# Performance work log

Hardware: AMD Instinct MI355X
Metric: run time of the kernel (lower is better)

The kernel has to match this reference:

```python
import math
import jax, jax.numpy as jnp
import numpy as np

T = 2048       # sequence_length
H = 2048       # hidden_size
NH = 32        # num_attention_heads
NKV = 8        # num_key_value_heads
HD = 64        # head_dim
SW = 128       # sliding_window
QM = NH // NKV # q_mult (GQA group size)
ROPE_THETA = 10000.0
EPS = 1e-5


def setup_inputs() -> dict:
    key = jax.random.key(0)
    k_x, k_s, k_qkv, k_out = jax.random.split(key, 4)
    x = jax.random.normal(k_x, (T, H), dtype=jnp.float32)
    scale = jnp.ones((H,), dtype=jnp.float32)
    sinks = jax.random.normal(k_s, (NH,), dtype=jnp.float32) * 0.02
    qkv_dim = HD * (NH + 2 * NKV)  # 3072
    qkv_kernel = jax.random.normal(k_qkv, (H, qkv_dim), dtype=jnp.float32) * (1.0 / math.sqrt(H))
    qkv_bias = jnp.zeros((qkv_dim,), dtype=jnp.float32)
    out_kernel = jax.random.normal(k_out, (H, H), dtype=jnp.float32) * (1.0 / math.sqrt(H))
    out_bias = jnp.zeros((H,), dtype=jnp.float32)
    # RoPE tables: [T, HD//2]
    half = HD // 2
    inv_freq = 1.0 / (ROPE_THETA ** (np.arange(half, dtype=np.float64) / half))
    ang = np.outer(np.arange(T, dtype=np.float64), inv_freq)
    cos_table = jnp.asarray(np.cos(ang), dtype=jnp.float32)
    sin_table = jnp.asarray(np.sin(ang), dtype=jnp.float32)
    # causal + sliding-window additive mask [T, T]
    qp = np.arange(T, dtype=np.int32)[:, None]
    kp = np.arange(T, dtype=np.int32)[None, :]
    m = np.where(kp > qp, -np.inf, 0.0) + np.where(qp - kp > SW, -np.inf, 0.0)
    mask = jnp.asarray(m, dtype=jnp.float32)
    return dict(x=x, scale=scale, sinks=sinks, qkv_kernel=qkv_kernel,
                qkv_bias=qkv_bias, out_kernel=out_kernel, out_bias=out_bias,
                cos_table=cos_table, sin_table=sin_table, mask=mask)


def _rmsnorm(x, scale):
    t = x.astype(jnp.float32)
    rms = jnp.sqrt(jnp.mean(t * t, axis=-1, keepdims=True) + EPS)
    return ((t / rms) * scale).astype(x.dtype)


def _rope(x, cos, sin):
    # x: [T, ..., HD]; split-half rotation as in the reference RotaryEmbedding
    shp = x.shape
    xr = x.reshape(shp[0], -1, HD)
    c = cos[:, None, :].astype(xr.dtype)
    s = sin[:, None, :].astype(xr.dtype)
    x1, x2 = jnp.split(xr, 2, axis=-1)
    y = jnp.concatenate([x1 * c - x2 * s, x2 * c + x1 * s], axis=-1)
    return y.reshape(shp)


def reference(x, scale, sinks, qkv_kernel, qkv_bias, out_kernel, out_bias,
              cos_table, sin_table, mask):
    normed = _rmsnorm(x, scale)
    qkv = normed @ qkv_kernel + qkv_bias                 # [T, 3072]
    q_end = NH * HD
    k_end = q_end + NKV * HD
    q = qkv[:, :q_end].reshape(T, NKV, QM, HD)           # [T, nkv, qm, hd]
    k = qkv[:, q_end:k_end].reshape(T, NKV, HD)          # [T, nkv, hd]
    v = qkv[:, k_end:].reshape(T, NKV, HD)               # [T, nkv, hd]
    q = _rope(q, cos_table, sin_table)
    k = _rope(k, cos_table, sin_table)
    sm_scale = 1.0 / math.sqrt(float(HD))
    # GQA attention without materializing repeated K/V
    logits = jnp.einsum('qnmd,knd->nmqk', q, k) * sm_scale  # [nkv, qm, T, T]
    logits = logits + mask[None, None, :, :]
    sink_col = jnp.broadcast_to(sinks.reshape(NKV, QM, 1, 1), (NKV, QM, T, 1))
    logits = jnp.concatenate([logits, sink_col], axis=-1)   # [nkv, qm, T, T+1]
    weights = jax.nn.softmax(logits, axis=-1)[..., :-1]     # drop sink column
    attn = jnp.einsum('nmqk,knd->qnmd', weights, v).reshape(T, NH * HD)
    projected = attn @ out_kernel + out_bias
    return x + projected
```

## Files before the change

### kernel.cpp

```cpp
#include <hip/hip_runtime.h>
#include <hip/hip_bf16.h>
#include <stdint.h>

typedef __bf16 bf16_t;
typedef __attribute__((ext_vector_type(8))) __bf16 bf16x8;
typedef __attribute__((ext_vector_type(4))) __bf16 bf16x4;
typedef __attribute__((ext_vector_type(4))) float f32x4;

static constexpr int T_SEQ = 2048;
static constexpr int HID   = 2048;
static constexpr int NHEAD = 32;
static constexpr int NKVH  = 8;
static constexpr int HDIM  = 64;
static constexpr int QKVD  = 3072;

__device__ inline f32x4 mfma16(bf16x8 a, bf16x8 b, f32x4 c) {
    return __builtin_amdgcn_mfma_f32_16x16x32_bf16(a, b, c, 0, 0, 0);
}

__device__ inline void load_lds16(const bf16_t* g, bf16_t* l) {
    __builtin_amdgcn_global_load_lds(
        (const __attribute__((address_space(1))) void*)g,
        (__attribute__((address_space(3))) void*)l, 16, 0, 0);
}

__global__ __launch_bounds__(256) void prep_kernel(const float* __restrict__ Wq,
                                                   const float* __restrict__ Wo,
                                                   bf16_t* __restrict__ Tq,
                                                   bf16_t* __restrict__ To,
                                                   const float* __restrict__ x,
                                                   const float* __restrict__ scale,
                                                   bf16_t* __restrict__ normed,
                                                   const float* __restrict__ obias,
                                                   float* __restrict__ out) {
    __shared__ float tile[64 * 65];
    int b = blockIdx.x;
    const int t = threadIdx.x;
    if (b < 2560) {
        const float* in; bf16_t* outw; int NN, KK, bx, by;
        if (b < 1536) { in = Wq; outw = Tq; NN = QKVD; KK = HID; bx = b % 48; by = b / 48; }
        else { b -= 1536; in = Wo; outw = To; NN = HID; KK = HID; bx = b % 32; by = b / 32; }
        const int c4 = (t & 15) * 4;
#pragma unroll
        for (int i = 0; i < 4; ++i) {
            int r = (t >> 4) + i * 16;
            float4 v = *(const float4*)(in + (size_t)(by*64 + r) * NN + bx*64 + c4);
            tile[r*65 + c4 + 0] = v.x; tile[r*65 + c4 + 1] = v.y;
            tile[r*65 + c4 + 2] = v.z; tile[r*65 + c4 + 3] = v.w;
        }
        __syncthreads();
        const int kc = t & 7;
#pragma unroll
        for (int i = 0; i < 2; ++i) {
            int n = (t >> 3) + i * 32;
            bf16x8 o;
#pragma unroll
            for (int j = 0; j < 8; ++j) o[j] = (bf16_t)tile[(kc*8 + j)*65 + n];
            *(bf16x8*)(outw + (size_t)(bx*64 + n) * KK + by*64 + kc*8) = o;
        }
    } else {
        int row = b - 2560;
        const float4* x4 = (const float4*)(x + (size_t)row * HID);
        const float4* s4 = (const float4*)scale;
        const float4* b4 = (const float4*)obias;
        float4 v0 = x4[t], v1 = x4[t + 256];
        float ss = v0.x*v0.x + v0.y*v0.y + v0.z*v0.z + v0.w*v0.w
                 + v1.x*v1.x + v1.y*v1.y + v1.z*v1.z + v1.w*v1.w;
#pragma unroll
        for (int off = 32; off > 0; off >>= 1) ss += __shfl_down(ss, off);
        if ((t & 63) == 0) tile[t >> 6] = ss;
        __syncthreads();
        float total = tile[0] + tile[1] + tile[2] + tile[3];
        float inv = rsqrtf(total * (1.0f / HID) + 1e-5f);
        float4 sc0 = s4[t], sc1 = s4[t + 256];
        bf16_t* outr = normed + (size_t)row * HID;
        bf16x4 o0, o1;
        o0.x = (bf16_t)(v0.x*inv*sc0.x); o0.y = (bf16_t)(v0.y*inv*sc0.y);
        o0.z = (bf16_t)(v0.z*inv*sc0.z); o0.w = (bf16_t)(v0.w*inv*sc0.w);
        o1.x = (bf16_t)(v1.x*inv*sc1.x); o1.y = (bf16_t)(v1.y*inv*sc1.y);
        o1.z = (bf16_t)(v1.z*inv*sc1.z); o1.w = (bf16_t)(v1.w*inv*sc1.w);
        *(bf16x4*)(outr + 4*t)        = o0;
        *(bf16x4*)(outr + 1024 + 4*t) = o1;
        float4 bb0 = b4[t], bb1 = b4[t + 256];
        float4 oi0 = {v0.x + bb0.x, v0.y + bb0.y, v0.z + bb0.z, v0.w + bb0.w};
        float4 oi1 = {v1.x + bb1.x, v1.y + bb1.y, v1.z + bb1.z, v1.w + bb1.w};
        float* orow = out + (size_t)row * HID;
        *(float4*)(orow + 4*t)        = oi0;
        *(float4*)(orow + 1024 + 4*t) = oi1;
    }
}

template <int ATOMIC>
__global__ __launch_bounds__(256) void gemm_splitk(const bf16_t* __restrict__ A,
                                                   const bf16_t* __restrict__ Bt,
                                                   bf16_t* __restrict__ Cpart,
                                                   float* __restrict__ Cred,
                                                   int M, int N, int K) {
    __shared__ __align__(16) bf16_t Asm[2 * 128 * 32];
    __shared__ __align__(16) bf16_t Bsm[2 * 128 * 32];
    const int tid = threadIdx.x;
    const int bm = blockIdx.y * 128, bn = blockIdx.x * 128;
    const int kh = K >> 1;
    const int kb = blockIdx.z * kh;
    const int lane = tid & 63, wave = tid >> 6;
    const int wm = (wave & 1) * 64, wn = (wave >> 1) * 64;
    const int lm = lane & 15, quad = lane >> 4;

    f32x4 acc[4][4];
#pragma unroll
    for (int i = 0; i < 4; ++i)
#pragma unroll
        for (int j = 0; j < 4; ++j) acc[i][j] = (f32x4){0.f, 0.f, 0.f, 0.f};

    const int cid0 = tid, cid1 = tid + 256;
    const int r0 = cid0 >> 2, c0 = (cid0 & 3) ^ ((r0 >> 1) & 3);
    const int r1 = cid1 >> 2, c1 = (cid1 & 3) ^ ((r1 >> 1) & 3);
    const bf16_t* Ab = A  + (size_t)bm * K + kb;
    const bf16_t* Bb = Bt + (size_t)bn * K + kb;
    const size_t ga0 = (size_t)r0 * K + c0 * 8;
    const size_t ga1 = (size_t)r1 * K + c1 * 8;
    bf16_t* ldsA0a = &Asm[wave * 512];
    bf16_t* ldsA0b = &Asm[2048 + wave * 512];
    bf16_t* ldsA1a = &Asm[4096 + wave * 512];
    bf16_t* ldsA1b = &Asm[4096 + 2048 + wave * 512];
    bf16_t* ldsB0a = &Bsm[wave * 512];
    bf16_t* ldsB0b = &Bsm[2048 + wave * 512];
    bf16_t* ldsB1a = &Bsm[4096 + wave * 512];
    bf16_t* ldsB1b = &Bsm[4096 + 2048 + wave * 512];
    const int swz = (quad ^ ((lm >> 1) & 3)) * 8;

    for (int k0 = 0; k0 < kh; k0 += 64) {
        load_lds16(Ab + ga0 + k0,      ldsA0a);
        load_lds16(Ab + ga1 + k0,      ldsA0b);
        load_lds16(Ab + ga0 + k0 + 32, ldsA1a);
        load_lds16(Ab + ga1 + k0 + 32, ldsA1b);
        load_lds16(Bb + ga0 + k0,      ldsB0a);
        load_lds16(Bb + ga1 + k0,      ldsB0b);
        load_lds16(Bb + ga0 + k0 + 32, ldsB1a);
        load_lds16(Bb + ga1 + k0 + 32, ldsB1b);
        __syncthreads();
#pragma unroll
        for (int ks = 0; ks < 2; ++ks) {
            bf16x8 af[4], bfr[4];
#pragma unroll
            for (int i = 0; i < 4; ++i)
                af[i]  = *(const bf16x8*)&Asm[ks*4096 + (wm + i*16 + lm)*32 + swz];
#pragma unroll
            for (int j = 0; j < 4; ++j)
                bfr[j] = *(const bf16x8*)&Bsm[ks*4096 + (wn + j*16 + lm)*32 + swz];
#pragma unroll
            for (int i = 0; i < 4; ++i)
#pragma unroll
                for (int j = 0; j < 4; ++j) acc[i][j] = mfma16(af[i], bfr[j], acc[i][j]);
        }
        __syncthreads();
    }

    if (ATOMIC) {
#pragma unroll
        for (int i = 0; i < 4; ++i) {
            int gr = bm + wm + i*16 + quad*4;
#pragma unroll
            for (int j = 0; j < 4; ++j) {
                int gc = bn + wn + j*16 + lm;
#pragma unroll
                for (int r = 0; r < 4; ++r)
                    atomicAdd(&Cred[(size_t)(gr + r)*N + gc], acc[i][j][r]);
            }
        }
    } else {
        bf16_t* Cp = Cpart + (size_t)blockIdx.z * M * N;
#pragma unroll
        for (int i = 0; i < 4; ++i) {
            int gr = bm + wm + i*16 + quad*4;
#pragma unroll
            for (int j = 0; j < 4; ++j) {
                int gc = bn + wn + j*16 + lm;
#pragma unroll
                for (int r = 0; r < 4; ++r)
                    Cp[(size_t)(gr + r)*N + gc] = (bf16_t)acc[i][j][r];
            }
        }
    }
}

__global__ __launch_bounds__(192) void rope_split(const bf16_t* __restrict__ qp0,
                                                  const bf16_t* __restrict__ qp1,
                                                  const float* __restrict__ qbias,
                                                  const float* __restrict__ cost,
                                                  const float* __restrict__ sint,
                                                  bf16_t* __restrict__ Qb,
                                                  bf16_t* __restrict__ Kb,
                                                  bf16_t* __restrict__ Vb) {
    const int t = blockIdx.x;
    const int hr = threadIdx.x >> 2, p0 = (threadIdx.x & 3) * 8;
    const bf16_t* r0 = qp0 + (size_t)t * QKVD + hr * 64;
    const bf16_t* r1 = qp1 + (size_t)t * QKVD + hr * 64;
    bf16x8 a1 = *(const bf16x8*)(r0 + p0);
    bf16x8 a2 = *(const bf16x8*)(r0 + p0 + 32);
    bf16x8 b1 = *(const bf16x8*)(r1 + p0);
    bf16x8 b2 = *(const bf16x8*)(r1 + p0 + 32);
    const float* qb = qbias + hr * 64;
    float x1[8], x2[8];
#pragma unroll
    for (int j = 0; j < 8; ++j) {
        x1[j] = (float)a1[j] + (float)b1[j] + qb[p0 + j];
        x2[j] = (float)a2[j] + (float)b2[j] + qb[p0 + j + 32];
    }
    bf16x8 w1, w2;
    if (hr < 40) {
        const float* c = cost + (size_t)t * 32 + p0;
        const float* s = sint + (size_t)t * 32 + p0;
#pragma unroll
        for (int j = 0; j < 8; ++j) {
            float cc = c[j], ss = s[j];
            w1[j] = (bf16_t)(x1[j]*cc - x2[j]*ss);
            w2[j] = (bf16_t)(x2[j]*cc + x1[j]*ss);
        }
    } else {
#pragma unroll
        for (int j = 0; j < 8; ++j) { w1[j] = (bf16_t)x1[j]; w2[j] = (bf16_t)x2[j]; }
    }
    bf16_t* dst;
    if (hr < 32)      dst = Qb + ((size_t)t*NHEAD + hr)      * HDIM;
    else if (hr < 40) dst = Kb + ((size_t)t*NKVH + (hr-32))  * HDIM;
    else              dst = Vb + ((size_t)t*NKVH + (hr-40))  * HDIM;
    *(bf16x8*)(dst + p0)      = w1;
    *(bf16x8*)(dst + p0 + 32) = w2;
}

__global__ __launch_bounds__(256) void attn_kernel(const bf16_t* __restrict__ Qb,
                                                   const bf16_t* __restrict__ Kb,
                                                   const bf16_t* __restrict__ Vb,
                                                   const float* __restrict__ sinks,
                                                   bf16_t* __restrict__ attnb) {
    __shared__ __align__(16) bf16_t Vt[64 * 200];
    __shared__ __align__(16) bf16_t Ws[64 * 200];

    const int tid = threadIdx.x;
    const int qt = blockIdx.x, h = blockIdx.y;
    const int qs = qt * 64;
    const int nkv = h >> 2;

    {
        const int off = (tid >> 5) * 8;
#pragma unroll
        for (int it = 0; it < 3; ++it) {
            int j2 = (tid & 31) + 32 * it;
            int kg0 = qs - 128 + 2*j2;     if (kg0 < 0) kg0 = 0;
            int kg1 = qs - 128 + 2*j2 + 1; if (kg1 < 0) kg1 = 0;
            union { uint4 u; bf16_t e[8]; } v0, v1;
            v0.u = *(const uint4*)(Vb + ((size_t)kg0*NKVH + nkv)*HDIM + off);
            v1.u = *(const uint4*)(Vb + ((size_t)kg1*NKVH + nkv)*HDIM + off);
#pragma unroll
            for (int r = 0; r < 8; ++r) {
                union { uint u; bf16_t e[2]; } p;
                p.e[0] = v0.e[r]; p.e[1] = v1.e[r];
                *(uint*)&Vt[(off + r)*200 + 2*j2] = p.u;
            }
        }
    }

    const int lane = tid & 63, wave = tid >> 6;
    const int lm = lane & 15, quad = lane >> 4;
    const int w16 = wave * 16;

    f32x4 S[12];
#pragma unroll
    for (int jt = 0; jt < 12; ++jt) S[jt] = (f32x4){0.f, 0.f, 0.f, 0.f};
    const bf16_t* Qrow = Qb + ((size_t)(qs + w16 + lm)*NHEAD + h)*HDIM + quad*8;
    int krow[12];
#pragma unroll
    for (int jt = 0; jt < 12; ++jt) {
        int kg = qs - 128 + jt*16 + lm;
        krow[jt] = kg < 0 ? 0 : kg;
    }
#pragma unroll
    for (int ks = 0; ks < 2; ++ks) {
        bf16x8 aq = *(const bf16x8*)(Qrow + ks*32);
#pragma unroll
        for (int jt = 0; jt < 12; ++jt) {
            bf16x8 bk = *(const bf16x8*)(Kb + ((size_t)krow[jt]*NKVH + nkv)*HDIM + ks*32 + quad*8);
            S[jt] = mfma16(aq, bk, S[jt]);
        }
    }

    const float sink = sinks[h];
#pragma unroll
    for (int reg = 0; reg < 4; ++reg) {
        const int qg = qs + w16 + quad*4 + reg;
        float mx = -1e30f;
#pragma unroll
        for (int jt = 0; jt < 12; ++jt) {
            int kg = qs - 128 + jt*16 + lm;
            float sv = S[jt][reg] * 0.125f;
            bool valid = (kg >= 0) && (kg <= qg) && (qg - kg <= 128);
            sv = valid ? sv : -1e30f;
            S[jt][reg] = sv;
            mx = fmaxf(mx, sv);
        }
#pragma unroll
        for (int off = 1; off < 16; off <<= 1) mx = fmaxf(mx, __shfl_xor(mx, off));
        float M = fmaxf(mx, sink);
        float sum = 0.f;
#pragma unroll
        for (int jt = 0; jt < 12; ++jt) {
            float e = __expf(S[jt][reg] - M);
            S[jt][reg] = e; sum += e;
        }
#pragma unroll
        for (int off = 1; off < 16; off <<= 1) sum += __shfl_xor(sum, off);
        float rden = 1.f / (sum + __expf(sink - M));
#pragma unroll
        for (int jt = 0; jt < 12; ++jt)
            Ws[(w16 + quad*4 + reg)*200 + jt*16 + lm] = (bf16_t)(S[jt][reg] * rden);
    }
    __syncthreads();

    f32x4 O[4];
#pragma unroll
    for (int nt = 0; nt < 4; ++nt) O[nt] = (f32x4){0.f, 0.f, 0.f, 0.f};
#pragma unroll
    for (int ks = 0; ks < 6; ++ks) {
        bf16x8 aw = *(const bf16x8*)&Ws[(w16 + lm)*200 + ks*32 + quad*8];
#pragma unroll
        for (int nt = 0; nt < 4; ++nt) {
            bf16x8 bv = *(const bf16x8*)&Vt[(nt*16 + lm)*200 + ks*32 + quad*8];
            O[nt] = mfma16(aw, bv, O[nt]);
        }
    }
#pragma unroll
    for (int nt = 0; nt < 4; ++nt)
#pragma unroll
        for (int reg = 0; reg < 4; ++reg)
            attnb[(size_t)(qs + w16 + quad*4 + reg)*HID + h*HDIM + nt*16 + lm] =
                (bf16_t)(O[nt][reg]);
}

extern "C" void kernel_launch(void* const* d_in, const int* in_sizes, int n_in,
                              void* d_out, int out_size, void* d_ws, size_t ws_size,
                              hipStream_t stream) {
    (void)in_sizes; (void)n_in; (void)out_size; (void)ws_size;
    const float* x          = (const float*)d_in[0];
    const float* scale      = (const float*)d_in[1];
    const float* sinks      = (const float*)d_in[2];
    const float* qkv_kernel = (const float*)d_in[3];
    const float* qkv_bias   = (const float*)d_in[4];
    const float* out_kernel = (const float*)d_in[5];
    const float* out_bias   = (const float*)d_in[6];
    const float* cos_t      = (const float*)d_in[7];
    const float* sin_t      = (const float*)d_in[8];
    float* out = (float*)d_out;

    char* ws = (char*)d_ws;
    const size_t MiB = 1048576;
    bf16_t* Wt_out = (bf16_t*)(ws);
    bf16_t* Wt_qkv = (bf16_t*)(ws + 8*MiB);
    bf16_t* attnb  = (bf16_t*)(ws + 8*MiB);
    bf16_t* normed = (bf16_t*)(ws + 20*MiB);
    bf16_t* qkvp   = (bf16_t*)(ws + 28*MiB);
    bf16_t* Qb     = (bf16_t*)(ws + 52*MiB);
    bf16_t* Kb     = (bf16_t*)(ws + 60*MiB);
    bf16_t* Vb     = (bf16_t*)(ws + 62*MiB);

    prep_kernel<<<4608, 256, 0, stream>>>(qkv_kernel, out_kernel, Wt_qkv, Wt_out,
                                          x, scale, normed, out_bias, out);
    gemm_splitk<0><<<dim3(QKVD/128, T_SEQ/128, 2), 256, 0, stream>>>(normed, Wt_qkv, qkvp,
                                                                     nullptr, T_SEQ, QKVD, HID);
    rope_split<<<T_SEQ, 192, 0, stream>>>(qkvp, qkvp + (size_t)T_SEQ*QKVD, qkv_bias,
                                          cos_t, sin_t, Qb, Kb, Vb);
    attn_kernel<<<dim3(T_SEQ/64, NHEAD), 256, 0, stream>>>(Qb, Kb, Vb, sinks, attnb);
    gemm_splitk<1><<<dim3(HID/128, T_SEQ/128, 2), 256, 0, stream>>>(attnb, Wt_out, nullptr,
                                                                    out, T_SEQ, HID, HID);
}
```

Measured before the change: 231.2 us.

## Fuse split-K reduction with RoPE/bias epilogues via per-tile flag handoff

```diff
diff --git a/kernel.cpp b/kernel.cpp
--- a/kernel.cpp
+++ b/kernel.cpp
@@ -23,6 +23,59 @@
         (const __attribute__((address_space(1))) void*)g,
         (__attribute__((address_space(3))) void*)l, 16, 0, 0);
 }
+
+#define GEMM_CORE(A_, Bt_, K_)                                                      \
+    const int tid = threadIdx.x;                                                    \
+    const int bm = blockIdx.y * 128, bn = blockIdx.x * 128;                         \
+    const int kh = (K_) >> 1;                                                       \
+    const int kb = blockIdx.z * kh;                                                 \
+    const int lane = tid & 63, wave = tid >> 6;                                     \
+    const int wm = (wave & 1) * 64, wn = (wave >> 1) * 64;                          \
+    const int lm = lane & 15, quad = lane >> 4;                                     \
+    f32x4 acc[4][4];                                                                \
+    _Pragma("unroll") for (int i = 0; i < 4; ++i)                                   \
+        _Pragma("unroll") for (int j = 0; j < 4; ++j)                               \
+            acc[i][j] = (f32x4){0.f, 0.f, 0.f, 0.f};                                \
+    {                                                                               \
+        const int cid0 = tid, cid1 = tid + 256;                                     \
+        const int r0 = cid0 >> 2, c0 = (cid0 & 3) ^ ((r0 >> 1) & 3);                \
+        const int r1 = cid1 >> 2, c1 = (cid1 & 3) ^ ((r1 >> 1) & 3);                \
+        const bf16_t* Ab = (A_)  + (size_t)bm * (K_) + kb;                          \
+        const bf16_t* Bb = (Bt_) + (size_t)bn * (K_) + kb;                          \
+        const size_t ga0 = (size_t)r0 * (K_) + c0 * 8;                              \
+        const size_t ga1 = (size_t)r1 * (K_) + c1 * 8;                              \
+        bf16_t* lA0a = &Asm[wave * 512];                                            \
+        bf16_t* lA0b = &Asm[2048 + wave * 512];                                     \
+        bf16_t* lA1a = &Asm[4096 + wave * 512];                                     \
+        bf16_t* lA1b = &Asm[6144 + wave * 512];                                     \
+        bf16_t* lB0a = &Bsm[wave * 512];                                            \
+        bf16_t* lB0b = &Bsm[2048 + wave * 512];                                     \
+        bf16_t* lB1a = &Bsm[4096 + wave * 512];                                     \
+        bf16_t* lB1b = &Bsm[6144 + wave * 512];                                     \
+        const int swz = (quad ^ ((lm >> 1) & 3)) * 8;                               \
+        for (int k0 = 0; k0 < kh; k0 += 64) {                                       \
+            load_lds16(Ab + ga0 + k0,      lA0a);                                   \
+            load_lds16(Ab + ga1 + k0,      lA0b);                                   \
+            load_lds16(Ab + ga0 + k0 + 32, lA1a);                                   \
+            load_lds16(Ab + ga1 + k0 + 32, lA1b);                                   \
+            load_lds16(Bb + ga0 + k0,      lB0a);                                   \
+            load_lds16(Bb + ga1 + k0,      lB0b);                                   \
+            load_lds16(Bb + ga0 + k0 + 32, lB1a);                                   \
+            load_lds16(Bb + ga1 + k0 + 32, lB1b);                                   \
+            __syncthreads();                                                        \
+            _Pragma("unroll") for (int ks = 0; ks < 2; ++ks) {                      \
+                bf16x8 af[4], bfr[4];                                               \
+                _Pragma("unroll") for (int i = 0; i < 4; ++i)                       \
+                    af[i]  = *(const bf16x8*)&Asm[ks*4096 + (wm + i*16 + lm)*32 + swz]; \
+                _Pragma("unroll") for (int j = 0; j < 4; ++j)                       \
+                    bfr[j] = *(const bf16x8*)&Bsm[ks*4096 + (wn + j*16 + lm)*32 + swz]; \
+                _Pragma("unroll") for (int i = 0; i < 4; ++i)                       \
+                    _Pragma("unroll") for (int j = 0; j < 4; ++j)                   \
+                        acc[i][j] = mfma16(af[i], bfr[j], acc[i][j]);               \
+            }                                                                       \
+            __syncthreads();                                                        \
+        }                                                                           \
+    }
 
 __global__ __launch_bounds__(256) void prep_kernel(const float* __restrict__ Wq,
                                                    const float* __restrict__ Wo,
@@ -31,11 +84,14 @@
                                                    const float* __restrict__ x,
                                                    const float* __restrict__ scale,
                                                    bf16_t* __restrict__ normed,
-                                                   const float* __restrict__ obias,
-                                                   float* __restrict__ out) {
+                                                   unsigned* __restrict__ flags) {
     __shared__ float tile[64 * 65];
     int b = blockIdx.x;
     const int t = threadIdx.x;
+    if (b == 4608) {
+        for (int i = t; i < 640; i += 256) flags[i] = 0u;
+        return;
+    }
     if (b < 2560) {
         const float* in; bf16_t* outw; int NN, KK, bx, by;
         if (b < 1536) { in = Wq; outw = Tq; NN = QKVD; KK = HID; bx = b % 48; by = b / 48; }
@@ -62,7 +118,6 @@
         int row = b - 2560;
         const float4* x4 = (const float4*)(x + (size_t)row * HID);
         const float4* s4 = (const float4*)scale;
-        const float4* b4 = (const float4*)obias;
         float4 v0 = x4[t], v1 = x4[t + 256];
         float ss = v0.x*v0.x + v0.y*v0.y + v0.z*v0.z + v0.w*v0.w
                  + v1.x*v1.x + v1.y*v1.y + v1.z*v1.z + v1.w*v1.w;
@@ -81,152 +136,137 @@
         o1.z = (bf16_t)(v1.z*inv*sc1.z); o1.w = (bf16_t)(v1.w*inv*sc1.w);
         *(bf16x4*)(outr + 4*t)        = o0;
         *(bf16x4*)(outr + 1024 + 4*t) = o1;
-        float4 bb0 = b4[t], bb1 = b4[t + 256];
-        float4 oi0 = {v0.x + bb0.x, v0.y + bb0.y, v0.z + bb0.z, v0.w + bb0.w};
-        float4 oi1 = {v1.x + bb1.x, v1.y + bb1.y, v1.z + bb1.z, v1.w + bb1.w};
-        float* orow = out + (size_t)row * HID;
-        *(float4*)(orow + 4*t)        = oi0;
-        *(float4*)(orow + 1024 + 4*t) = oi1;
-    }
-}
-
-template <int ATOMIC>
-__global__ __launch_bounds__(256) void gemm_splitk(const bf16_t* __restrict__ A,
-                                                   const bf16_t* __restrict__ Bt,
-                                                   bf16_t* __restrict__ Cpart,
-                                                   float* __restrict__ Cred,
-                                                   int M, int N, int K) {
+    }
+}
+
+__global__ __launch_bounds__(256) void gemm_qkv(const bf16_t* __restrict__ A,
+                                                const bf16_t* __restrict__ Bt,
+                                                bf16_t* __restrict__ P,
+                                                unsigned* __restrict__ flags,
+                                                const float* __restrict__ qbias,
+                                                const float* __restrict__ cost,
+                                                const float* __restrict__ sint,
+                                                bf16_t* __restrict__ Qb,
+                                                bf16_t* __restrict__ Kb,
+                                                bf16_t* __restrict__ Vb) {
     __shared__ __align__(16) bf16_t Asm[2 * 128 * 32];
     __shared__ __align__(16) bf16_t Bsm[2 * 128 * 32];
-    const int tid = threadIdx.x;
-    const int bm = blockIdx.y * 128, bn = blockIdx.x * 128;
-    const int kh = K >> 1;
-    const int kb = blockIdx.z * kh;
-    const int lane = tid & 63, wave = tid >> 6;
-    const int wm = (wave & 1) * 64, wn = (wave >> 1) * 64;
-    const int lm = lane & 15, quad = lane >> 4;
-
-    f32x4 acc[4][4];
-#pragma unroll
-    for (int i = 0; i < 4; ++i)
-#pragma unroll
-        for (int j = 0; j < 4; ++j) acc[i][j] = (f32x4){0.f, 0.f, 0.f, 0.f};
-
-    const int cid0 = tid, cid1 = tid + 256;
-    const int r0 = cid0 >> 2, c0 = (cid0 & 3) ^ ((r0 >> 1) & 3);
-    const int r1 = cid1 >> 2, c1 = (cid1 & 3) ^ ((r1 >> 1) & 3);
-    const bf16_t* Ab = A  + (size_t)bm * K + kb;
-    const bf16_t* Bb = Bt + (size_t)bn * K + kb;
-    const size_t ga0 = (size_t)r0 * K + c0 * 8;
-    const size_t ga1 = (size_t)r1 * K + c1 * 8;
-    bf16_t* ldsA0a = &Asm[wave * 512];
-    bf16_t* ldsA0b = &Asm[2048 + wave * 512];
-    bf16_t* ldsA1a = &Asm[4096 + wave * 512];
-    bf16_t* ldsA1b = &Asm[4096 + 2048 + wave * 512];
-    bf16_t* ldsB0a = &Bsm[wave * 512];
-    bf16_t* ldsB0b = &Bsm[2048 + wave * 512];
-    bf16_t* ldsB1a = &Bsm[4096 + wave * 512];
-    bf16_t* ldsB1b = &Bsm[4096 + 2048 + wave * 512];
-    const int swz = (quad ^ ((lm >> 1) & 3)) * 8;
-
-    for (int k0 = 0; k0 < kh; k0 += 64) {
-        load_lds16(Ab + ga0 + k0,      ldsA0a);
-        load_lds16(Ab + ga1 + k0,      ldsA0b);
-        load_lds16(Ab + ga0 + k0 + 32, ldsA1a);
-        load_lds16(Ab + ga1 + k0 + 32, ldsA1b);
-        load_lds16(Bb + ga0 + k0,      ldsB0a);
-        load_lds16(Bb + ga1 + k0,      ldsB0b);
-        load_lds16(Bb + ga0 + k0 + 32, ldsB1a);
-        load_lds16(Bb + ga1 + k0 + 32, ldsB1b);
-        __syncthreads();
-#pragma unroll
-        for (int ks = 0; ks < 2; ++ks) {
-            bf16x8 af[4], bfr[4];
-#pragma unroll
-            for (int i = 0; i < 4; ++i)
-                af[i]  = *(const bf16x8*)&Asm[ks*4096 + (wm + i*16 + lm)*32 + swz];
+    __shared__ unsigned s_role;
+    GEMM_CORE(A, Bt, HID)
+
+    const int tilei = blockIdx.y * gridDim.x + blockIdx.x;
+    unsigned* flag = flags + tilei;
+    bf16_t* Pt = P + (size_t)tilei * 16384;
+    if (tid == 0) s_role = atomicAdd(flag, 1u);
+    __syncthreads();
+    if (s_role == 0) {
+#pragma unroll
+        for (int i = 0; i < 4; ++i)
+#pragma unroll
+            for (int j = 0; j < 4; ++j) {
+                bf16x4 v;
+#pragma unroll
+                for (int r = 0; r < 4; ++r) v[r] = (bf16_t)acc[i][j][r];
+                *(bf16x4*)(Pt + wave*4096 + (i*4 + j)*256 + lane*4) = v;
+            }
+        __syncthreads();
+        if (tid == 0) { __threadfence(); atomicAdd(flag, 4u); }
+    } else {
+        if (tid == 0) { while (atomicAdd(flag, 0u) < 5u) __builtin_amdgcn_s_sleep(2); }
+        __syncthreads();
+        __threadfence();
+        const int hr = (bn + wn) >> 6;
+        float bcol[4];
+#pragma unroll
+        for (int j = 0; j < 4; ++j) bcol[j] = qbias[bn + wn + j*16 + lm];
+#pragma unroll
+        for (int i = 0; i < 4; ++i) {
+            bf16x4 pv[4];
 #pragma unroll
             for (int j = 0; j < 4; ++j)
-                bfr[j] = *(const bf16x8*)&Bsm[ks*4096 + (wn + j*16 + lm)*32 + swz];
-#pragma unroll
-            for (int i = 0; i < 4; ++i)
-#pragma unroll
-                for (int j = 0; j < 4; ++j) acc[i][j] = mfma16(af[i], bfr[j], acc[i][j]);
-        }
-        __syncthreads();
-    }
-
-    if (ATOMIC) {
+                pv[j] = *(const bf16x4*)(Pt + wave*4096 + (i*4 + j)*256 + lane*4);
+#pragma unroll
+            for (int r = 0; r < 4; ++r) {
+                const int t = bm + wm + i*16 + quad*4 + r;
+                float v0 = acc[i][0][r] + (float)pv[0][r] + bcol[0];
+                float v1 = acc[i][1][r] + (float)pv[1][r] + bcol[1];
+                float v2 = acc[i][2][r] + (float)pv[2][r] + bcol[2];
+                float v3 = acc[i][3][r] + (float)pv[3][r] + bcol[3];
+                bf16_t o0, o1, o2, o3;
+                if (hr < 40) {
+                    float c0 = cost[t*32 + lm],      s0 = sint[t*32 + lm];
+                    float c1 = cost[t*32 + 16 + lm], s1 = sint[t*32 + 16 + lm];
+                    o0 = (bf16_t)(v0*c0 - v2*s0);
+                    o1 = (bf16_t)(v1*c1 - v3*s1);
+                    o2 = (bf16_t)(v2*c0 + v0*s0);
+                    o3 = (bf16_t)(v3*c1 + v1*s1);
+                } else {
+                    o0 = (bf16_t)v0; o1 = (bf16_t)v1; o2 = (bf16_t)v2; o3 = (bf16_t)v3;
+                }
+                bf16_t* dst;
+                if (hr < 32)      dst = Qb + ((size_t)t*NHEAD + hr)      * HDIM;
+                else if (hr < 40) dst = Kb + ((size_t)t*NKVH + (hr-32))  * HDIM;
+                else              dst = Vb + ((size_t)t*NKVH + (hr-40))  * HDIM;
+                dst[lm] = o0; dst[16 + lm] = o1; dst[32 + lm] = o2; dst[48 + lm] = o3;
+            }
+        }
+    }
+}
+
+__global__ __launch_bounds__(256) void gemm_out(const bf16_t* __restrict__ A,
+                                                const bf16_t* __restrict__ Bt,
+                                                bf16_t* __restrict__ P,
+                                                unsigned* __restrict__ flags,
+                                                const float* __restrict__ obias,
+                                                const float* __restrict__ x,
+                                                float* __restrict__ out) {
+    __shared__ __align__(16) bf16_t Asm[2 * 128 * 32];
+    __shared__ __align__(16) bf16_t Bsm[2 * 128 * 32];
+    __shared__ unsigned s_role;
+    GEMM_CORE(A, Bt, HID)
+
+    const int tilei = blockIdx.y * gridDim.x + blockIdx.x;
+    unsigned* flag = flags + tilei;
+    bf16_t* Pt = P + (size_t)tilei * 16384;
+    if (tid == 0) s_role = atomicAdd(flag, 1u);
+    __syncthreads();
+    if (s_role == 0) {
+#pragma unroll
+        for (int i = 0; i < 4; ++i)
+#pragma unroll
+            for (int j = 0; j < 4; ++j) {
+                bf16x4 v;
+#pragma unroll
+                for (int r = 0; r < 4; ++r) v[r] = (bf16_t)acc[i][j][r];
+                *(bf16x4*)(Pt + wave*4096 + (i*4 + j)*256 + lane*4) = v;
+            }
+        __syncthreads();
+        if (tid == 0) { __threadfence(); atomicAdd(flag, 4u); }
+    } else {
+        if (tid == 0) { while (atomicAdd(flag, 0u) < 5u) __builtin_amdgcn_s_sleep(2); }
+        __syncthreads();
+        __threadfence();
+        float bcol[4];
+#pragma unroll
+        for (int j = 0; j < 4; ++j) bcol[j] = obias[bn + wn + j*16 + lm];
 #pragma unroll
         for (int i = 0; i < 4; ++i) {
-            int gr = bm + wm + i*16 + quad*4;
-#pragma unroll
-            for (int j = 0; j < 4; ++j) {
-                int gc = bn + wn + j*16 + lm;
-#pragma unroll
-                for (int r = 0; r < 4; ++r)
-                    atomicAdd(&Cred[(size_t)(gr + r)*N + gc], acc[i][j][r]);
+            bf16x4 pv[4];
+#pragma unroll
+            for (int j = 0; j < 4; ++j)
+                pv[j] = *(const bf16x4*)(Pt + wave*4096 + (i*4 + j)*256 + lane*4);
+#pragma unroll
+            for (int r = 0; r < 4; ++r) {
+                const int t = bm + wm + i*16 + quad*4 + r;
+#pragma unroll
+                for (int j = 0; j < 4; ++j) {
+                    const int gc = bn + wn + j*16 + lm;
+                    out[(size_t)t*HID + gc] = acc[i][j][r] + (float)pv[j][r] + bcol[j]
+                                            + x[(size_t)t*HID + gc];
+                }
             }
         }
-    } else {
-        bf16_t* Cp = Cpart + (size_t)blockIdx.z * M * N;
-#pragma unroll
-        for (int i = 0; i < 4; ++i) {
-            int gr = bm + wm + i*16 + quad*4;
-#pragma unroll
-            for (int j = 0; j < 4; ++j) {
-                int gc = bn + wn + j*16 + lm;
-#pragma unroll
-                for (int r = 0; r < 4; ++r)
-                    Cp[(size_t)(gr + r)*N + gc] = (bf16_t)acc[i][j][r];
-            }
-        }
-    }
-}
-
-__global__ __launch_bounds__(192) void rope_split(const bf16_t* __restrict__ qp0,
-                                                  const bf16_t* __restrict__ qp1,
-                                                  const float* __restrict__ qbias,
-                                                  const float* __restrict__ cost,
-                                                  const float* __restrict__ sint,
-                                                  bf16_t* __restrict__ Qb,
-                                                  bf16_t* __restrict__ Kb,
-                                                  bf16_t* __restrict__ Vb) {
-    const int t = blockIdx.x;
-    const int hr = threadIdx.x >> 2, p0 = (threadIdx.x & 3) * 8;
-    const bf16_t* r0 = qp0 + (size_t)t * QKVD + hr * 64;
-    const bf16_t* r1 = qp1 + (size_t)t * QKVD + hr * 64;
-    bf16x8 a1 = *(const bf16x8*)(r0 + p0);
-    bf16x8 a2 = *(const bf16x8*)(r0 + p0 + 32);
-    bf16x8 b1 = *(const bf16x8*)(r1 + p0);
-    bf16x8 b2 = *(const bf16x8*)(r1 + p0 + 32);
-    const float* qb = qbias + hr * 64;
-    float x1[8], x2[8];
-#pragma unroll
-    for (int j = 0; j < 8; ++j) {
-        x1[j] = (float)a1[j] + (float)b1[j] + qb[p0 + j];
-        x2[j] = (float)a2[j] + (float)b2[j] + qb[p0 + j + 32];
-    }
-    bf16x8 w1, w2;
-    if (hr < 40) {
-        const float* c = cost + (size_t)t * 32 + p0;
-        const float* s = sint + (size_t)t * 32 + p0;
-#pragma unroll
-        for (int j = 0; j < 8; ++j) {
-            float cc = c[j], ss = s[j];
-            w1[j] = (bf16_t)(x1[j]*cc - x2[j]*ss);
-            w2[j] = (bf16_t)(x2[j]*cc + x1[j]*ss);
-        }
-    } else {
-#pragma unroll
-        for (int j = 0; j < 8; ++j) { w1[j] = (bf16_t)x1[j]; w2[j] = (bf16_t)x2[j]; }
-    }
-    bf16_t* dst;
-    if (hr < 32)      dst = Qb + ((size_t)t*NHEAD + hr)      * HDIM;
-    else if (hr < 40) dst = Kb + ((size_t)t*NKVH + (hr-32))  * HDIM;
-    else              dst = Vb + ((size_t)t*NKVH + (hr-40))  * HDIM;
-    *(bf16x8*)(dst + p0)      = w1;
-    *(bf16x8*)(dst + p0 + 32) = w2;
+    }
 }
 
 __global__ __launch_bounds__(256) void attn_kernel(const bf16_t* __restrict__ Qb,
@@ -254,9 +294,9 @@
             v1.u = *(const uint4*)(Vb + ((size_t)kg1*NKVH + nkv)*HDIM + off);
 #pragma unroll
             for (int r = 0; r < 8; ++r) {
-                union { uint u; bf16_t e[2]; } p;
-                p.e[0] = v0.e[r]; p.e[1] = v1.e[r];
-                *(uint*)&Vt[(off + r)*200 + 2*j2] = p.u;
+                union { uint u; bf16_t e[2]; } pp;
+                pp.e[0] = v0.e[r]; pp.e[1] = v1.e[r];
+                *(uint*)&Vt[(off + r)*200 + 2*j2] = pp.u;
             }
         }
     }
@@ -354,22 +394,22 @@
 
     char* ws = (char*)d_ws;
     const size_t MiB = 1048576;
-    bf16_t* Wt_out = (bf16_t*)(ws);
-    bf16_t* Wt_qkv = (bf16_t*)(ws + 8*MiB);
-    bf16_t* attnb  = (bf16_t*)(ws + 8*MiB);
-    bf16_t* normed = (bf16_t*)(ws + 20*MiB);
-    bf16_t* qkvp   = (bf16_t*)(ws + 28*MiB);
-    bf16_t* Qb     = (bf16_t*)(ws + 52*MiB);
-    bf16_t* Kb     = (bf16_t*)(ws + 60*MiB);
-    bf16_t* Vb     = (bf16_t*)(ws + 62*MiB);
-
-    prep_kernel<<<4608, 256, 0, stream>>>(qkv_kernel, out_kernel, Wt_qkv, Wt_out,
-                                          x, scale, normed, out_bias, out);
-    gemm_splitk<0><<<dim3(QKVD/128, T_SEQ/128, 2), 256, 0, stream>>>(normed, Wt_qkv, qkvp,
-                                                                     nullptr, T_SEQ, QKVD, HID);
-    rope_split<<<T_SEQ, 192, 0, stream>>>(qkvp, qkvp + (size_t)T_SEQ*QKVD, qkv_bias,
-                                          cos_t, sin_t, Qb, Kb, Vb);
+    bf16_t* Wt_out  = (bf16_t*)(ws);
+    bf16_t* Wt_qkv  = (bf16_t*)(ws + 8*MiB);
+    bf16_t* attnb   = (bf16_t*)(ws + 8*MiB);
+    bf16_t* normed  = (bf16_t*)(ws + 20*MiB);
+    bf16_t* Pq      = (bf16_t*)(ws + 28*MiB);
+    bf16_t* Po      = (bf16_t*)(ws + 40*MiB);
+    unsigned* flags = (unsigned*)(ws + 48*MiB);
+    bf16_t* Qb      = (bf16_t*)(ws + 52*MiB);
+    bf16_t* Kb      = (bf16_t*)(ws + 60*MiB);
+    bf16_t* Vb      = (bf16_t*)(ws + 62*MiB);
+
+    prep_kernel<<<4609, 256, 0, stream>>>(qkv_kernel, out_kernel, Wt_qkv, Wt_out,
+                                          x, scale, normed, flags);
+    gemm_qkv<<<dim3(QKVD/128, T_SEQ/128, 2), 256, 0, stream>>>(
+        normed, Wt_qkv, Pq, flags, qkv_bias, cos_t, sin_t, Qb, Kb, Vb);
     attn_kernel<<<dim3(T_SEQ/64, NHEAD), 256, 0, stream>>>(Qb, Kb, Vb, sinks, attnb);
-    gemm_splitk<1><<<dim3(HID/128, T_SEQ/128, 2), 256, 0, stream>>>(attnb, Wt_out, nullptr,
-                                                                    out, T_SEQ, HID, HID);
-}
+    gemm_out<<<dim3(HID/128, T_SEQ/128, 2), 256, 0, stream>>>(
+        attnb, Wt_out, Po, flags + 384, out_bias, x, out);
+}
```

Measured after the change: 290.5 us. +25.7%, slower.
